# Optimization experiments

Hardware: AMD Instinct MI355X
Metric: run time of the kernel (lower is better)

The kernel has to match this reference:

```python
import jax, jax.numpy as jnp
import numpy as np

LN_EPS = 1e-5


def _gru_scan(xg, w_hh, b_hh, H, reverse):
    # xg: [T, B, 3H] precomputed input-gate activations (W_ih x + b_ih)
    B = xg.shape[1]
    h0 = jnp.zeros((B, H), xg.dtype)

    def step(h, xt):
        hg = h @ w_hh.T + b_hh                      # [B, 3H]
        r = jax.nn.sigmoid(xt[:, :H] + hg[:, :H])
        z = jax.nn.sigmoid(xt[:, H:2 * H] + hg[:, H:2 * H])
        n = jnp.tanh(xt[:, 2 * H:] + r * hg[:, 2 * H:])
        h = (1.0 - z) * n + z * h
        return h, h

    _, ys = jax.lax.scan(step, h0, xg, reverse=reverse)
    return ys                                       # [T, B, H]


def setup_inputs() -> dict:
    key = jax.random.key(0)
    ks = jax.random.split(key, 12)
    B, T, I, H = 32, 1000, 512, 512
    s = 1.0 / np.sqrt(H)
    u = lambda k, shape: jax.random.uniform(k, shape, jnp.float32, -s, s)
    return {
        "x": jax.random.normal(ks[0], (B, T, I), jnp.float32),
        "ln_gamma": jnp.ones((I,), jnp.float32),
        "ln_beta": jnp.zeros((I,), jnp.float32),
        "w_ih_f": u(ks[1], (3 * H, I)),
        "w_hh_f": u(ks[2], (3 * H, H)),
        "b_ih_f": u(ks[3], (3 * H,)),
        "b_hh_f": u(ks[4], (3 * H,)),
        "w_ih_b": u(ks[5], (3 * H, I)),
        "w_hh_b": u(ks[6], (3 * H, H)),
        "b_ih_b": u(ks[7], (3 * H,)),
        "b_hh_b": u(ks[8], (3 * H,)),
    }


def reference(x, ln_gamma, ln_beta, w_ih_f, w_hh_f, b_ih_f, b_hh_f,
              w_ih_b, w_hh_b, b_ih_b, b_hh_b):
    H = w_hh_f.shape[1]
    # LayerNorm over last dim
    mu = jnp.mean(x, axis=-1, keepdims=True)
    var = jnp.var(x, axis=-1, keepdims=True)
    xn = (x - mu) * jax.lax.rsqrt(var + LN_EPS) * ln_gamma + ln_beta
    # ReLU6
    xn = jnp.clip(xn, 0.0, 6.0)
    # batch_first -> time-major [T, B, I]
    xt = jnp.transpose(xn, (1, 0, 2))
    # Precompute input projections for both directions
    xg_f = xt @ w_ih_f.T + b_ih_f                   # [T, B, 3H]
    xg_b = xt @ w_ih_b.T + b_ih_b
    yf = _gru_scan(xg_f, w_hh_f, b_hh_f, H, reverse=False)
    yb = _gru_scan(xg_b, w_hh_b, b_hh_b, H, reverse=True)
    y = jnp.concatenate([yf, yb], axis=-1)          # [T, B, 2H]
    # dropout treated as identity (deterministic reference)
    return jnp.transpose(y, (1, 0, 2))              # [B, T, 2H]
```

## Files before the change

kernel.cpp:

```cpp
#include <hip/hip_runtime.h>


typedef _Float16 half8   __attribute__((ext_vector_type(8)));
typedef _Float16 half2_  __attribute__((ext_vector_type(2)));
typedef float    floatx4 __attribute__((ext_vector_type(4)));
typedef float    floatx2 __attribute__((ext_vector_type(2)));
typedef unsigned int uintx4 __attribute__((ext_vector_type(4)));

#define T_LEN 1000
#define DIM   512

#define XN_OFF   0
#define HT_OFF   32768000
#define FLAG_OFF 32899072
#define WS_NEED  32903168

__device__ __forceinline__ float bf2f(unsigned short b) {
  unsigned int u = ((unsigned int)b) << 16; float f; __builtin_memcpy(&f, &u, 4); return f;
}
__device__ __forceinline__ unsigned short f2bf(float f) {
  unsigned int u; __builtin_memcpy(&u, &f, 4);
  u = (u + 0x7FFFu + ((u >> 16) & 1u)) >> 16;
  return (unsigned short)u;
}

__global__ void init_kernel(unsigned long long* ws64) {
  const int base = HT_OFF / 8;
  const int n    = (WS_NEED - HT_OFF) / 8;
  for (int i = blockIdx.x * blockDim.x + threadIdx.x; i < n; i += gridDim.x * blockDim.x)
    ws64[base + i] = 0ull;
}

__global__ __launch_bounds__(256) void ln_kernel(const void* __restrict__ xin,
                                                 const void* __restrict__ gam,
                                                 const void* __restrict__ bet,
                                                 unsigned short* __restrict__ xn) {
  const bool bf = (((const unsigned int*)gam)[0] != 0x3F800000u);
  const int w = threadIdx.x >> 6, l = threadIdx.x & 63;
  const int row = blockIdx.x * 4 + w;
  const int b = row / T_LEN, t = row - b * T_LEN;

  float v[8], g[8], be[8];
  if (bf) {
    const unsigned int* xp = (const unsigned int*)xin + (row * 512 + l * 8) / 2;
    uintx4 r4 = *(const uintx4*)xp;
    uintx4 g4 = *(const uintx4*)((const unsigned int*)gam + l * 4);
    uintx4 b4 = *(const uintx4*)((const unsigned int*)bet + l * 4);
#pragma unroll
    for (int j = 0; j < 4; ++j) {
      v[2*j]   = bf2f((unsigned short)(r4[j] & 0xFFFFu));
      v[2*j+1] = bf2f((unsigned short)(r4[j] >> 16));
      g[2*j]   = bf2f((unsigned short)(g4[j] & 0xFFFFu));
      g[2*j+1] = bf2f((unsigned short)(g4[j] >> 16));
      be[2*j]  = bf2f((unsigned short)(b4[j] & 0xFFFFu));
      be[2*j+1] = bf2f((unsigned short)(b4[j] >> 16));
    }
  } else {
    const float* xp = (const float*)xin + (size_t)row * 512 + l * 8;
    floatx4 a0 = *(const floatx4*)xp;
    floatx4 a1 = *(const floatx4*)(xp + 4);
    const float* gp = (const float*)gam + l * 8;
    const float* bp = (const float*)bet + l * 8;
#pragma unroll
    for (int j = 0; j < 4; ++j) {
      v[j] = a0[j]; v[4+j] = a1[j];
      g[j] = gp[j]; g[4+j] = gp[4+j];
      be[j] = bp[j]; be[4+j] = bp[4+j];
    }
  }

  float s1 = 0.f, s2 = 0.f;
#pragma unroll
  for (int j = 0; j < 8; ++j) { s1 += v[j]; s2 += v[j] * v[j]; }
#pragma unroll
  for (int m = 1; m < 64; m <<= 1) { s1 += __shfl_xor(s1, m); s2 += __shfl_xor(s2, m); }
  const float mean = s1 * (1.f / 512.f);
  const float var  = s2 * (1.f / 512.f) - mean * mean;
  const float rstd = rsqrtf(var + 1e-5f);

  unsigned int out[4];
#pragma unroll
  for (int j = 0; j < 4; ++j) {
    float f0 = (v[2*j]   - mean) * rstd * g[2*j]   + be[2*j];
    float f1 = (v[2*j+1] - mean) * rstd * g[2*j+1] + be[2*j+1];
    f0 = fminf(fmaxf(f0, 0.f), 6.f);
    f1 = fminf(fmaxf(f1, 0.f), 6.f);
    half2_ hp = { (_Float16)f0, (_Float16)f1 };
    __builtin_memcpy(&out[j], &hp, 4);
  }
  *(uintx4*)(xn + ((size_t)(t * 32 + b) * 512 + l * 8)) = *(uintx4*)out;
}

#define SMEM_BYTES 52608
#define TILE_F 272
#define PBUF_F 6528

__global__ __launch_bounds__(256, 1) void gru_kernel(
    const void* __restrict__ wihF, const void* __restrict__ whhF,
    const void* __restrict__ bihF, const void* __restrict__ bhhF,
    const void* __restrict__ wihB, const void* __restrict__ whhB,
    const void* __restrict__ bihB, const void* __restrict__ bhhB,
    const void* __restrict__ gam,
    const unsigned short* __restrict__ xn,
    unsigned int* __restrict__ hb,
    unsigned int* __restrict__ flags,
    void* __restrict__ yout) {
  extern __shared__ char smem[];
  float* part = (float*)smem;
  float* bihs = (float*)(smem + 52224);
  float* bhhs = (float*)(smem + 52416);

  const bool bf = (((const unsigned int*)gam)[0] != 0x3F800000u);
  const int tid = threadIdx.x;
  const int w = tid >> 6, l = tid & 63, quad = l >> 4, lan = l & 15;
  const int dir = blockIdx.x >> 5, wg = blockIdx.x & 31, c0 = wg * 16;
  const int kh = w & 1;

  const void* Wih = dir ? wihB : wihF;
  const void* Whh = dir ? whhB : whhF;
  const void* Bih = dir ? bihB : bihF;
  const void* Bhh = dir ? bhhB : bhhF;

  half8 wfrag[3][8];
  {
    const void* Wm = (w < 2) ? Wih : Whh;
    const int col = c0 + lan;
    const int kq  = quad * 8;
#pragma unroll
    for (int nt = 0; nt < 3; ++nt)
#pragma unroll
      for (int si = 0; si < 8; ++si) {
        const int s = kh * 8 + si;
        const int row = nt * 512 + col;
        const int k0 = s * 32 + kq;
        half8 hh;
        if (bf) {
          const unsigned int* p = (const unsigned int*)Wm + (row * 512 + k0) / 2;
          uintx4 r4 = *(const uintx4*)p;
#pragma unroll
          for (int j = 0; j < 4; ++j) {
            hh[2*j]   = (_Float16)bf2f((unsigned short)(r4[j] & 0xFFFFu));
            hh[2*j+1] = (_Float16)bf2f((unsigned short)(r4[j] >> 16));
          }
        } else {
          const float* p = (const float*)Wm + (size_t)row * 512 + k0;
          floatx4 a0 = *(const floatx4*)p;
          floatx4 a1 = *(const floatx4*)(p + 4);
#pragma unroll
          for (int j = 0; j < 4; ++j) { hh[j] = (_Float16)a0[j]; hh[4+j] = (_Float16)a1[j]; }
        }
        wfrag[nt][si] = hh;
      }
  }

  if (tid < 96) {
    const int mat = tid / 48, i = tid % 48, g_ = i >> 4, c = i & 15;
    const int gi = g_ * 512 + c0 + c;
    const void* Bm = mat ? Bhh : Bih;
    float v = bf ? bf2f(((const unsigned short*)Bm)[gi]) : ((const float*)Bm)[gi];
    (mat ? bhhs : bihs)[i] = v;
  }

  const int cb = tid >> 3, cp = tid & 7, cmt = cb >> 4, cmr = cb & 15;
  float hpv0 = 0.f, hpv1 = 0.f;

  unsigned int* hbD   = hb + dir * 16384;
  unsigned int* flagD = flags + dir * 512;

  const int p_s   = wg >> 1;
  const int p_q   = (wg & 1) * 2 + (cp >> 2);
  const int p_hs  = (cp >> 1) & 1;
  const int p_widx = (p_s * 2 + cmt) * 256 + p_hs * 128 + (p_q * 16 + cmr) * 2 + (cp & 1);

  for (int t = 0; t < T_LEN; ++t) {
    const int tt = dir ? (T_LEN - 1 - t) : t;
    float* pb = part + (t & 1) * PBUF_F;

    floatx4 acc[2][3];
#pragma unroll
    for (int mt = 0; mt < 2; ++mt)
#pragma unroll
      for (int nt = 0; nt < 3; ++nt) acc[mt][nt] = (floatx4){0.f, 0.f, 0.f, 0.f};

    if (w < 2) {
      const _Float16* A = (const _Float16*)xn + (size_t)tt * 16384;
      half8 av0[8], av1[8];
#pragma unroll
      for (int si = 0; si < 8; ++si) {
        const int k0 = (kh * 8 + si) * 32 + quad * 8;
        av0[si] = *(const half8*)(A + (lan * 512 + k0));
        av1[si] = *(const half8*)(A + ((16 + lan) * 512 + k0));
      }
#pragma unroll
      for (int si = 0; si < 8; ++si)
#pragma unroll
        for (int nt = 0; nt < 3; ++nt) {
          acc[0][nt] = __builtin_amdgcn_mfma_f32_16x16x32_f16(av0[si], wfrag[nt][si], acc[0][nt], 0, 0, 0);
          acc[1][nt] = __builtin_amdgcn_mfma_f32_16x16x32_f16(av1[si], wfrag[nt][si], acc[1][nt], 0, 0, 0);
        }
    } else {
      const unsigned int tgt = (unsigned int)t;
      while (true) {
        unsigned int hv = tgt;
        if (l < 16)
          hv = __hip_atomic_load(flagD + (kh * 16 + l) * 16,
                                 __ATOMIC_RELAXED, __HIP_MEMORY_SCOPE_AGENT);
        if (__all((int)(hv >= tgt)) != 0) break;
        __builtin_amdgcn_s_sleep(2);
      }
      asm volatile("" ::: "memory");

      const unsigned long long* h64 =
          (const unsigned long long*)(hbD + (t & 1) * 8192);
      unsigned long long q[32];
#pragma unroll
      for (int si = 0; si < 8; ++si) {
        const int cA = kh * 16 + si * 2;
#pragma unroll
        for (int mt = 0; mt < 2; ++mt) {
          const unsigned long long* p = h64 + (size_t)(cA + mt) * 128 + l;
          q[(si * 2 + mt) * 2 + 0] = __hip_atomic_load(p,      __ATOMIC_RELAXED, __HIP_MEMORY_SCOPE_AGENT);
          q[(si * 2 + mt) * 2 + 1] = __hip_atomic_load(p + 64, __ATOMIC_RELAXED, __HIP_MEMORY_SCOPE_AGENT);
        }
      }
#pragma unroll
      for (int si = 0; si < 8; ++si)
#pragma unroll
        for (int mt = 0; mt < 2; ++mt) {
          union HU { unsigned long long u[2]; half8 h; } a;
          a.u[0] = q[(si * 2 + mt) * 2 + 0];
          a.u[1] = q[(si * 2 + mt) * 2 + 1];
#pragma unroll
          for (int nt = 0; nt < 3; ++nt)
            acc[mt][nt] = __builtin_amdgcn_mfma_f32_16x16x32_f16(a.h, wfrag[nt][si], acc[mt][nt], 0, 0, 0);
        }
    }

#pragma unroll
    for (int mt = 0; mt < 2; ++mt)
#pragma unroll
      for (int nt = 0; nt < 3; ++nt) {
        float* p = pb + (w * 6 + mt * 3 + nt) * TILE_F;
#pragma unroll
        for (int r = 0; r < 4; ++r) p[(quad * 4 + r) * 17 + lan] = acc[mt][nt][r];
      }

    __builtin_amdgcn_sched_barrier(0);
    asm volatile("s_waitcnt lgkmcnt(0)" ::: "memory");
    __builtin_amdgcn_s_barrier();
    __builtin_amdgcn_sched_barrier(0);

    float hv[2];
#pragma unroll
    for (int e = 0; e < 2; ++e) {
      const int c = cp * 2 + e;
      const int o = cmr * 17 + c;
#define PT(W_, NT_) pb[(((W_) * 6 + cmt * 3 + (NT_)) * TILE_F) + o]
      const float xr = PT(0, 0) + PT(1, 0) + bihs[c];
      const float xz = PT(0, 1) + PT(1, 1) + bihs[16 + c];
      const float xg = PT(0, 2) + PT(1, 2) + bihs[32 + c];
      const float hr = PT(2, 0) + PT(3, 0) + bhhs[c];
      const float hz = PT(2, 1) + PT(3, 1) + bhhs[16 + c];
      const float hg = PT(2, 2) + PT(3, 2) + bhhs[32 + c];
#undef PT
      const float rr = 1.f / (1.f + __expf(-(xr + hr)));
      const float zz = 1.f / (1.f + __expf(-(xz + hz)));
      float a = xg + rr * hg;
      a = fminf(fmaxf(a, -15.f), 15.f);
      const float e2 = __expf(2.f * a);
      const float nn = (e2 - 1.f) / (e2 + 1.f);
      const float hp = e ? hpv1 : hpv0;
      const float hvv = (1.f - zz) * nn + zz * hp;
      if (e) hpv1 = hvv; else hpv0 = hvv;
      hv[e] = hvv;
    }

    if (t + 1 < T_LEN) {
      half2_ pk = { (_Float16)hv[0], (_Float16)hv[1] };
      unsigned int pu; __builtin_memcpy(&pu, &pk, 4);
      __hip_atomic_store(hbD + ((t + 1) & 1) * 8192 + p_widx, pu,
                         __ATOMIC_RELAXED, __HIP_MEMORY_SCOPE_AGENT);
      asm volatile("s_waitcnt vmcnt(0)" ::: "memory");
      __builtin_amdgcn_s_barrier();
      asm volatile("" ::: "memory");
      if (tid == 0)
        __hip_atomic_store(flagD + wg * 16, (unsigned int)(t + 1),
                           __ATOMIC_RELAXED, __HIP_MEMORY_SCOPE_AGENT);
    }

    {
      const size_t yo = ((size_t)cb * T_LEN + tt) * 1024 + dir * 512 + c0 + cp * 2;
      if (bf) {
        unsigned int yp = (unsigned int)f2bf(hv[0]) | ((unsigned int)f2bf(hv[1]) << 16);
        *(unsigned int*)((unsigned short*)yout + yo) = yp;
      } else {
        *(floatx2*)((float*)yout + yo) = (floatx2){hv[0], hv[1]};
      }
    }
  }
}

extern "C" void kernel_launch(void* const* d_in, const int* in_sizes, int n_in,
                              void* d_out, int out_size, void* d_ws, size_t ws_size,
                              hipStream_t stream) {
  if (ws_size < (size_t)WS_NEED) return;

  (void)hipFuncSetAttribute((const void*)gru_kernel,
                            hipFuncAttributeMaxDynamicSharedMemorySize, 65536);

  const void* x   = d_in[0];
  const void* gam = d_in[1];
  const void* bet = d_in[2];
  const void* wihF = d_in[3]; const void* whhF = d_in[4];
  const void* bihF = d_in[5]; const void* bhhF = d_in[6];
  const void* wihB = d_in[7]; const void* whhB = d_in[8];
  const void* bihB = d_in[9]; const void* bhhB = d_in[10];

  unsigned short* xnp   = (unsigned short*)((char*)d_ws + XN_OFF);
  unsigned int*   hbp   = (unsigned int*)((char*)d_ws + HT_OFF);
  unsigned int*   flagp = (unsigned int*)((char*)d_ws + FLAG_OFF);

  init_kernel<<<17, 256, 0, stream>>>((unsigned long long*)d_ws);
  ln_kernel<<<8000, 256, 0, stream>>>(x, gam, bet, xnp);
  gru_kernel<<<64, 256, SMEM_BYTES, stream>>>(wihF, whhF, bihF, bhhF,
                                              wihB, whhB, bihB, bhhB,
                                              gam, xnp, hbp, flagp, d_out);
}
```

Before: 4.505 ms.

## Replace per-step flag barrier with timestamp-tagged hidden-state words

Each published hidden-state value is now packed into a 64-bit word with the step counter in the upper half, so consumers spin directly on the data and check every tag, and the separate flag array is dropped. This removes the vmcnt wait, the block barrier and the flag store/poll round-trip on the recurrent critical path. In exchange the hidden-state buffer doubles in size, each consumer issues twice as many loads per step, and MFMA work is redone whenever a poll sees stale data.

```diff
diff --git a/kernel.cpp b/kernel.cpp
--- a/kernel.cpp
+++ b/kernel.cpp
@@ -12,8 +12,7 @@
 
 #define XN_OFF   0
 #define HT_OFF   32768000
-#define FLAG_OFF 32899072
-#define WS_NEED  32903168
+#define WS_NEED  33030144
 
 __device__ __forceinline__ float bf2f(unsigned short b) {
   unsigned int u = ((unsigned int)b) << 16; float f; __builtin_memcpy(&f, &u, 4); return f;
@@ -102,8 +101,7 @@
     const void* __restrict__ bihB, const void* __restrict__ bhhB,
     const void* __restrict__ gam,
     const unsigned short* __restrict__ xn,
-    unsigned int* __restrict__ hb,
-    unsigned int* __restrict__ flags,
+    unsigned long long* __restrict__ hb,
     void* __restrict__ yout) {
   extern __shared__ char smem[];
   float* part = (float*)smem;
@@ -164,25 +162,24 @@
   const int cb = tid >> 3, cp = tid & 7, cmt = cb >> 4, cmr = cb & 15;
   float hpv0 = 0.f, hpv1 = 0.f;
 
-  unsigned int* hbD   = hb + dir * 16384;
-  unsigned int* flagD = flags + dir * 512;
-
-  const int p_s   = wg >> 1;
-  const int p_q   = (wg & 1) * 2 + (cp >> 2);
-  const int p_hs  = (cp >> 1) & 1;
-  const int p_widx = (p_s * 2 + cmt) * 256 + p_hs * 128 + (p_q * 16 + cmr) * 2 + (cp & 1);
+  unsigned long long* hbD = hb + (size_t)dir * 16384;
+
+  const int p_s  = wg >> 1;
+  const int p_q  = (wg & 1) * 2 + (cp >> 2);
+  const int p_hs = (cp >> 1) & 1;
+  const int p_widx = (p_s * 2 + cmt) * 256 + p_hs * 128 + (cp & 1) * 64 + (p_q * 16 + cmr);
 
   for (int t = 0; t < T_LEN; ++t) {
     const int tt = dir ? (T_LEN - 1 - t) : t;
     float* pb = part + (t & 1) * PBUF_F;
 
     floatx4 acc[2][3];
-#pragma unroll
-    for (int mt = 0; mt < 2; ++mt)
-#pragma unroll
-      for (int nt = 0; nt < 3; ++nt) acc[mt][nt] = (floatx4){0.f, 0.f, 0.f, 0.f};
 
     if (w < 2) {
+#pragma unroll
+      for (int mt = 0; mt < 2; ++mt)
+#pragma unroll
+        for (int nt = 0; nt < 3; ++nt) acc[mt][nt] = (floatx4){0.f, 0.f, 0.f, 0.f};
       const _Float16* A = (const _Float16*)xn + (size_t)tt * 16384;
       half8 av0[8], av1[8];
 #pragma unroll
@@ -199,41 +196,36 @@
           acc[1][nt] = __builtin_amdgcn_mfma_f32_16x16x32_f16(av1[si], wfrag[nt][si], acc[1][nt], 0, 0, 0);
         }
     } else {
+      const unsigned long long* hbuf = hbD + (size_t)(t & 1) * 8192;
       const unsigned int tgt = (unsigned int)t;
       while (true) {
-        unsigned int hv = tgt;
-        if (l < 16)
-          hv = __hip_atomic_load(flagD + (kh * 16 + l) * 16,
-                                 __ATOMIC_RELAXED, __HIP_MEMORY_SCOPE_AGENT);
-        if (__all((int)(hv >= tgt)) != 0) break;
-        __builtin_amdgcn_s_sleep(2);
-      }
-      asm volatile("" ::: "memory");
-
-      const unsigned long long* h64 =
-          (const unsigned long long*)(hbD + (t & 1) * 8192);
-      unsigned long long q[32];
-#pragma unroll
-      for (int si = 0; si < 8; ++si) {
-        const int cA = kh * 16 + si * 2;
-#pragma unroll
-        for (int mt = 0; mt < 2; ++mt) {
-          const unsigned long long* p = h64 + (size_t)(cA + mt) * 128 + l;
-          q[(si * 2 + mt) * 2 + 0] = __hip_atomic_load(p,      __ATOMIC_RELAXED, __HIP_MEMORY_SCOPE_AGENT);
-          q[(si * 2 + mt) * 2 + 1] = __hip_atomic_load(p + 64, __ATOMIC_RELAXED, __HIP_MEMORY_SCOPE_AGENT);
+        unsigned int bad = 0u;
+#pragma unroll
+        for (int mt = 0; mt < 2; ++mt)
+#pragma unroll
+          for (int nt = 0; nt < 3; ++nt) acc[mt][nt] = (floatx4){0.f, 0.f, 0.f, 0.f};
+#pragma unroll
+        for (int si = 0; si < 8; ++si) {
+#pragma unroll
+          for (int mt = 0; mt < 2; ++mt) {
+            const int chunk = kh * 16 + si * 2 + mt;
+            const unsigned long long* p = hbuf + (size_t)chunk * 256 + l;
+            unsigned long long q0 = __hip_atomic_load(p,       __ATOMIC_RELAXED, __HIP_MEMORY_SCOPE_AGENT);
+            unsigned long long q1 = __hip_atomic_load(p + 64,  __ATOMIC_RELAXED, __HIP_MEMORY_SCOPE_AGENT);
+            unsigned long long q2 = __hip_atomic_load(p + 128, __ATOMIC_RELAXED, __HIP_MEMORY_SCOPE_AGENT);
+            unsigned long long q3 = __hip_atomic_load(p + 192, __ATOMIC_RELAXED, __HIP_MEMORY_SCOPE_AGENT);
+            bad |= (((unsigned int)(q0 >> 32)) ^ tgt) | (((unsigned int)(q1 >> 32)) ^ tgt)
+                 | (((unsigned int)(q2 >> 32)) ^ tgt) | (((unsigned int)(q3 >> 32)) ^ tgt);
+            union HU { unsigned int d[4]; half8 h; } a;
+            a.d[0] = (unsigned int)q0; a.d[1] = (unsigned int)q1;
+            a.d[2] = (unsigned int)q2; a.d[3] = (unsigned int)q3;
+#pragma unroll
+            for (int nt = 0; nt < 3; ++nt)
+              acc[mt][nt] = __builtin_amdgcn_mfma_f32_16x16x32_f16(a.h, wfrag[nt][si], acc[mt][nt], 0, 0, 0);
+          }
         }
-      }
-#pragma unroll
-      for (int si = 0; si < 8; ++si)
-#pragma unroll
-        for (int mt = 0; mt < 2; ++mt) {
-          union HU { unsigned long long u[2]; half8 h; } a;
-          a.u[0] = q[(si * 2 + mt) * 2 + 0];
-          a.u[1] = q[(si * 2 + mt) * 2 + 1];
-#pragma unroll
-          for (int nt = 0; nt < 3; ++nt)
-            acc[mt][nt] = __builtin_amdgcn_mfma_f32_16x16x32_f16(a.h, wfrag[nt][si], acc[mt][nt], 0, 0, 0);
-        }
+        if (__all((int)(bad == 0u)) != 0) break;
+      }
     }
 
 #pragma unroll
@@ -278,14 +270,10 @@
     if (t + 1 < T_LEN) {
       half2_ pk = { (_Float16)hv[0], (_Float16)hv[1] };
       unsigned int pu; __builtin_memcpy(&pu, &pk, 4);
-      __hip_atomic_store(hbD + ((t + 1) & 1) * 8192 + p_widx, pu,
+      const unsigned long long qv =
+          (unsigned long long)pu | ((unsigned long long)(unsigned int)(t + 1) << 32);
+      __hip_atomic_store(hbD + (size_t)((t + 1) & 1) * 8192 + p_widx, qv,
                          __ATOMIC_RELAXED, __HIP_MEMORY_SCOPE_AGENT);
-      asm volatile("s_waitcnt vmcnt(0)" ::: "memory");
-      __builtin_amdgcn_s_barrier();
-      asm volatile("" ::: "memory");
-      if (tid == 0)
-        __hip_atomic_store(flagD + wg * 16, (unsigned int)(t + 1),
-                           __ATOMIC_RELAXED, __HIP_MEMORY_SCOPE_AGENT);
     }
 
     {
@@ -316,13 +304,12 @@
   const void* wihB = d_in[7]; const void* whhB = d_in[8];
   const void* bihB = d_in[9]; const void* bhhB = d_in[10];
 
-  unsigned short* xnp   = (unsigned short*)((char*)d_ws + XN_OFF);
-  unsigned int*   hbp   = (unsigned int*)((char*)d_ws + HT_OFF);
-  unsigned int*   flagp = (unsigned int*)((char*)d_ws + FLAG_OFF);
-
-  init_kernel<<<17, 256, 0, stream>>>((unsigned long long*)d_ws);
+  unsigned short*     xnp = (unsigned short*)((char*)d_ws + XN_OFF);
+  unsigned long long* hbp = (unsigned long long*)((char*)d_ws + HT_OFF);
+
+  init_kernel<<<32, 256, 0, stream>>>((unsigned long long*)d_ws);
   ln_kernel<<<8000, 256, 0, stream>>>(x, gam, bet, xnp);
   gru_kernel<<<64, 256, SMEM_BYTES, stream>>>(wihF, whhF, bihF, bhhF,
                                               wihB, whhB, bihB, bhhB,
-                                              gam, xnp, hbp, flagp, d_out);
-}
+                                              gam, xnp, hbp, d_out);
+}
```

After: 5.541 ms. +23.0%, slower.
